# Performance work log

Hardware: AMD Instinct MI355X
Metric: run time of the kernel (lower is better)

The kernel has to match this reference:

```python
import jax, jax.numpy as jnp
from jax import lax
import numpy as np

# Problem dims (see init_kwargs)
B, CIN, H, W = 4, 128, 128, 128
COUT, K, STRIDE, PAD, DIL, GROUPS, OG = 128, 3, 1, 1, 1, 1, 2


def setup_inputs() -> dict:
    key = jax.random.key(0)
    k0, k1, k2 = jax.random.split(key, 3)
    x = jax.random.normal(k0, (B, CIN, H, W), dtype=jnp.float32)
    off_ch = 3 * OG * K * K  # with_mask=True -> scale=3 (dy, dx, mask)
    # Small random offset-conv weights so offsets are non-trivial (zero-init would degenerate to plain conv)
    w_off = jax.random.normal(k1, (off_ch, CIN, K, K), dtype=jnp.float32) * 0.01
    b_off = jnp.zeros((off_ch,), jnp.float32)
    stdv = 1.0 / np.sqrt(CIN * K * K)
    weight = jax.random.uniform(k2, (COUT, CIN // GROUPS, K, K), jnp.float32, -stdv, stdv)
    bias = jnp.zeros((COUT,), jnp.float32)
    return {"x": x, "w_off": w_off, "b_off": b_off, "weight": weight, "bias": bias}


def _deform_conv2d(x, offset, mask, weight, bias):
    # x: [B,C,H,W]; offset: [B,2*OG*K2,Ho,Wo]; mask: [B,OG*K2,Ho,Wo]
    Bn, C, Hn, Wn = x.shape
    O = weight.shape[0]
    K2 = K * K
    Ho = (Hn + 2 * PAD - DIL * (K - 1) - 1) // STRIDE + 1
    Wo = (Wn + 2 * PAD - DIL * (K - 1) - 1) // STRIDE + 1
    # torchvision layout: per offset group, per kernel point, (dy, dx) interleaved
    off = offset.reshape(Bn, OG, K2, 2, Ho, Wo)
    kg = (jnp.arange(K) * DIL).astype(x.dtype)
    kyf = jnp.repeat(kg, K)  # [K2] kernel row offset, k2 = i*K + j
    kxf = jnp.tile(kg, K)    # [K2] kernel col offset
    base_y = (jnp.arange(Ho) * STRIDE - PAD).astype(x.dtype)
    base_x = (jnp.arange(Wo) * STRIDE - PAD).astype(x.dtype)
    # sampling coords: [B,OG,K2,Ho,Wo]
    sy = base_y[None, None, None, :, None] + kyf[None, None, :, None, None] + off[:, :, :, 0]
    sx = base_x[None, None, None, None, :] + kxf[None, None, :, None, None] + off[:, :, :, 1]
    y0f = jnp.floor(sy)
    x0f = jnp.floor(sx)
    ly = sy - y0f  # bilinear fractional weights
    lx = sx - x0f
    y0 = y0f.astype(jnp.int32)
    x0 = x0f.astype(jnp.int32)
    Cg = C // OG
    xg = x.reshape(Bn, OG, Cg, Hn * Wn)

    def gather(iy, ix):
        # zero-padding semantics: out-of-range corners contribute 0
        valid = ((iy >= 0) & (iy < Hn) & (ix >= 0) & (ix < Wn)).astype(x.dtype)
        idx = (jnp.clip(iy, 0, Hn - 1) * Wn + jnp.clip(ix, 0, Wn - 1)).reshape(Bn, OG, 1, -1)
        v = jnp.take_along_axis(xg, idx, axis=3).reshape(Bn, OG, Cg, K2, Ho, Wo)
        return v * valid[:, :, None]

    v00 = gather(y0, x0)
    v01 = gather(y0, x0 + 1)
    v10 = gather(y0 + 1, x0)
    v11 = gather(y0 + 1, x0 + 1)
    wy = ly[:, :, None]  # broadcast over channel dim
    wx = lx[:, :, None]
    val = (v00 * (1 - wy) * (1 - wx) + v01 * (1 - wy) * wx
           + v10 * wy * (1 - wx) + v11 * wy * wx)
    # modulated DCNv2: multiply sampled values by sigmoid mask
    val = val * mask.reshape(Bn, OG, 1, K2, Ho, Wo)
    # im2col GEMM: cols [B,G,(C/G)*K2,Ho*Wo] x weight [G,O/G,(C/G)*K2]
    cols = val.reshape(Bn, GROUPS, (C // GROUPS) * K2, Ho * Wo)
    wg = weight.reshape(GROUPS, O // GROUPS, (C // GROUPS) * K2)
    out = jnp.einsum('gok,bgkn->bgon', wg, cols).reshape(Bn, O, Ho, Wo)
    return out + bias[None, :, None, None]


def reference(x, w_off, b_off, weight, bias):
    off_out = lax.conv_general_dilated(
        x, w_off, (STRIDE, STRIDE), [(PAD, PAD), (PAD, PAD)],
        rhs_dilation=(DIL, DIL), dimension_numbers=('NCHW', 'OIHW', 'NCHW')
    ) + b_off[None, :, None, None]
    oh, ow, m = jnp.split(off_out, 3, axis=1)
    offset = jnp.concatenate([oh, ow], axis=1)
    mask = jax.nn.sigmoid(m)
    return _deform_conv2d(x, offset, mask, weight, bias)
```

## Files before the change

### kernel.cpp

```cpp
#include <hip/hip_runtime.h>
#include <math.h>

#define NB 4
#define NC 128
#define NH 128
#define NW 128
#define NHW (NH*NW)
#define NCOUT 128

#define SY_OFF 0
#define SX_OFF 1179648
#define MK_OFF 2359296
#define WOFF_OFF 3538944
#define WMAIN_OFF 3580416
#define XT_OFF 3663360

typedef short short8 __attribute__((ext_vector_type(8)));
typedef float f32x4 __attribute__((ext_vector_type(4)));
typedef float f32x2 __attribute__((ext_vector_type(2)));

__device__ inline short f2bf(float f) {
    unsigned u = __float_as_uint(f);
    u = (u + 0x7FFFu + ((u >> 16) & 1u)) >> 16;
    return (short)u;
}
__device__ inline unsigned pack2(float lo, float hi) {
    unsigned r;
    asm("v_cvt_pk_bf16_f32 %0, %1, %2" : "=v"(r) : "v"(lo), "v"(hi));
    return r;
}
__device__ inline unsigned pkf16(float a, float b) {
    auto h = __builtin_amdgcn_cvt_pkrtz(a, b);
    unsigned r; __builtin_memcpy(&r, &h, 4); return r;
}
__device__ inline float f16f(unsigned s) {
    unsigned short us = (unsigned short)s;
    __fp16 h; __builtin_memcpy(&h, &us, 2); return (float)h;
}
__device__ inline f32x2 pkmul(f32x2 a, f32x2 b) {
    f32x2 d; asm("v_pk_mul_f32 %0, %1, %2" : "=v"(d) : "v"(a), "v"(b)); return d;
}
__device__ inline f32x2 pkfma(f32x2 a, f32x2 b, f32x2 c) {
    f32x2 d; asm("v_pk_fma_f32 %0, %1, %2, %3" : "=v"(d) : "v"(a), "v"(b), "v"(c)); return d;
}
__device__ inline f32x2 cpair(unsigned u) {
    f32x2 c; c.x = __uint_as_float(u << 16); c.y = __uint_as_float(u); return c;
}
__device__ inline void gload_lds16(const void* g, void* l) {
    __builtin_amdgcn_global_load_lds(
        (const __attribute__((address_space(1))) unsigned int*)g,
        (__attribute__((address_space(3))) unsigned int*)l, 16, 0, 0);
}

__global__ void wtrans_kernel(const float* __restrict__ w_off,
                              const float* __restrict__ weight,
                              float* __restrict__ ws)
{
    int i = blockIdx.x * 256 + threadIdx.x;
    if (i < 36*2304) {
        int s = i / 2304, rem = i - s*2304;
        int row = rem / 36, c = rem - row*36;
        int chunk = s / 9, k2 = s - 9*chunk;
        float v = (row < 54 && c < 32) ? w_off[(row*NC + chunk*32 + c)*9 + k2] : 0.f;
        ((short*)(ws + WOFF_OFF))[i] = f2bf(v);
    } else if (i < 36*2304 + 36*4608) {
        int j = i - 36*2304;
        int s = j / 4608, rem = j - s*4608;
        int row = rem / 36, c = rem - row*36;
        int chunk = s / 9, k2 = s - 9*chunk;
        float v = (c < 32) ? weight[(row*NC + chunk*32 + c)*9 + k2] : 0.f;
        ((short*)(ws + WMAIN_OFF))[j] = f2bf(v);
    }
}

__global__ __launch_bounds__(256) void xtrans_kernel(
    const float* __restrict__ x, float* __restrict__ ws)
{
    short* xT = (short*)(ws + XT_OFF);
    const int bid = blockIdx.x;
    const int ys = bid & 15, cg = (bid >> 4) & 15, b = bid >> 8;
    const int col = threadIdx.x & 127, rr = threadIdx.x >> 7;
    const float* xb = x + ((long)(b*NC + cg*8))*NHW;
#pragma unroll
    for (int yy = 0; yy < 4; ++yy) {
        const int y = ys*8 + yy*2 + rr;
        const float* p = xb + y*NW + col;
        float v[8];
#pragma unroll
        for (int q = 0; q < 8; ++q) v[q] = p[q*NHW];
        uint4 u = make_uint4(pack2(v[0],v[1]), pack2(v[2],v[3]),
                             pack2(v[4],v[5]), pack2(v[6],v[7]));
        *(uint4*)&xT[(((long)(b*16+cg)*NH + y)*NW + col)*8] = u;
    }
}

__global__ __launch_bounds__(512, 4) void offconv_kernel(
    float* __restrict__ ws, const float* __restrict__ b_off)
{
    __shared__ short wslab[2][2304];
    int bid = blockIdx.x;
    bid = (bid & 7) * 64 + (bid >> 3);
    const int b   = bid >> 7;
    const int ho  = bid & 127;
    const int tid = threadIdx.x;
    const int lane = tid & 63;
    const int wid = tid >> 6;
    const int n = lane & 15, g = lane >> 4;
    const int px = wid*16 + n;
    const short* woff = (const short*)(ws + WOFF_OFF);
    const char*  xTb  = (const char*)((const short*)(ws + XT_OFF) + (long)b*16*NHW*8);

    f32x4 acc[4];
#pragma unroll
    for (int rf = 0; rf < 4; ++rf) acc[rf] = (f32x4){0.f,0.f,0.f,0.f};

    auto DMA = [&](int it, int buf) {
        if (tid < 288) gload_lds16(woff + it*2304 + tid*8, &wslab[buf][tid*8]);
    };
    auto LOADB = [&](int it) -> short8 {
        const int chunk = it/9, k2 = it - 9*chunk;
        const int y = ho + k2/3 - 1, xc = px + (k2%3) - 1;
        short8 bf = (short8){0,0,0,0,0,0,0,0};
        if ((unsigned)y < NH && (unsigned)xc < NW)
            bf = *(const short8*)(xTb + ((long)(chunk*4 + g)*NHW + y*NW + xc)*16);
        return bf;
    };

    DMA(0, 0);
    short8 bcur = LOADB(0);
    asm volatile("s_waitcnt vmcnt(1) lgkmcnt(0)" ::: "memory");
    __builtin_amdgcn_s_barrier();
    __builtin_amdgcn_sched_barrier(0);

#pragma unroll 1
    for (int it = 0; it < 36; ++it) {
        const int cur = it & 1, nxt = cur ^ 1;
        short8 bnext;
        if (it < 35) { DMA(it+1, nxt); bnext = LOADB(it+1); }
        __builtin_amdgcn_sched_barrier(0);
#pragma unroll
        for (int rf = 0; rf < 4; ++rf) {
            short8 af = *(const short8*)&wslab[cur][(rf*16 + n)*36 + 8*g];
            acc[rf] = __builtin_amdgcn_mfma_f32_16x16x32_bf16(af, bcur, acc[rf], 0,0,0);
        }
        __builtin_amdgcn_sched_barrier(0);
        if (it < 35) {
            asm volatile("s_waitcnt vmcnt(1) lgkmcnt(0)" ::: "memory");
            __builtin_amdgcn_s_barrier();
            __builtin_amdgcn_sched_barrier(0);
        }
        bcur = bnext;
    }

#pragma unroll
    for (int rf = 0; rf < 4; ++rf) {
#pragma unroll
        for (int r = 0; r < 4; ++r) {
            int cout = 16*rf + 4*g + r;
            if (cout >= 54) continue;
            float v = acc[rf][r] + b_off[cout];
            if (cout < 36) {
                int og = cout / 18, rem = cout - 18*og;
                int k2c = rem >> 1, d = cout & 1;
                float base = d ? (float)(px - 1 + (k2c % 3))
                              : (float)(ho - 1 + (k2c / 3));
                ws[(d ? SX_OFF : SY_OFF) + (((b*2+og)*9 + k2c)*NHW) + ho*NW + px] = v + base;
            } else {
                int cc = cout - 36;
                int og = cc / 9, k2c = cc - 9*og;
                ws[MK_OFF + (((b*2+og)*9 + k2c)*NHW) + ho*NW + px] = 1.f/(1.f+expf(-v));
            }
        }
    }
}

__global__ __launch_bounds__(512, 4) void deform_kernel(
    float* __restrict__ ws, const float* __restrict__ bias,
    float* __restrict__ out)
{
    __shared__ short4 pI[18][128];
    __shared__ uint2  pWp[18][128];
    __shared__ short  wslab[2][4608];

    int bid = blockIdx.x;
    bid = (bid & 7) * 64 + (bid >> 3);
    const int b   = bid >> 7;
    const int ho  = bid & 127;
    const int tid = threadIdx.x;
    const int lane = tid & 63;
    const int wid = tid >> 6;
    const int n = lane & 15, g = lane >> 4;
    const int pxl = 16*wid + n;
    const short* wmn = (const short*)(ws + WMAIN_OFF);
    const char*  xTb = (const char*)((const short*)(ws + XT_OFF) + (long)b*16*NHW*8);

    f32x4 acc[8];
#pragma unroll
    for (int rf = 0; rf < 8; ++rf) acc[rf] = (f32x4){0.f,0.f,0.f,0.f};

    auto DMA = [&](int slabIdx, int buf) {
        const short* src = wmn + slabIdx*4608;
        gload_lds16(src + tid*8, &wslab[buf][tid*8]);
        if (tid < 64) gload_lds16(src + 4096 + tid*8, &wslab[buf][4096 + tid*8]);
    };

#define GLOAD(j, G0, G1, G2, G3) do {                                   \
        const int row_ = ((j)/18)*9 + (j)%9;                            \
        const int chunk_ = (j)/9;                                       \
        const short4 I_ = pI[row_][pxl];                                \
        const char* xp_ = xTb + (long)(chunk_*4 + g)*(NHW*16);          \
        G0 = *(const uint4*)(xp_ + (((int)I_.x) << 4));                 \
        G1 = *(const uint4*)(xp_ + (((int)I_.y) << 4));                 \
        G2 = *(const uint4*)(xp_ + (((int)I_.z) << 4));                 \
        G3 = *(const uint4*)(xp_ + (((int)I_.w) << 4));                 \
    } while (0)

#define FIN(j, G0, G1, G2, G3, Adst) do {                               \
        const int row_ = ((j)/18)*9 + (j)%9;                            \
        const uint2 wp_ = *(const uint2*)&pWp[row_][pxl];               \
        const float w0s = f16f(wp_.x), w1s = f16f(wp_.x >> 16);         \
        const float w2s = f16f(wp_.y), w3s = f16f(wp_.y >> 16);         \
        const f32x2 W0_ = {w0s, w0s}, W1_ = {w1s, w1s};                 \
        const f32x2 W2_ = {w2s, w2s}, W3_ = {w3s, w3s};                 \
        uint4 u_; unsigned* up_ = (unsigned*)&u_;                       \
        const unsigned* a_ = (const unsigned*)&G0;                      \
        const unsigned* b_ = (const unsigned*)&G1;                      \
        const unsigned* c_ = (const unsigned*)&G2;                      \
        const unsigned* d_ = (const unsigned*)&G3;                      \
        _Pragma("unroll")                                               \
        for (int e = 0; e < 4; ++e) {                                   \
            f32x2 r_ = pkmul(cpair(d_[e]), W3_);                        \
            r_ = pkfma(cpair(c_[e]), W2_, r_);                          \
            r_ = pkfma(cpair(b_[e]), W1_, r_);                          \
            r_ = pkfma(cpair(a_[e]), W0_, r_);                          \
            up_[e] = pack2(r_.x, r_.y);                                 \
        }                                                               \
        __builtin_memcpy(&Adst, &u_, 16);                               \
    } while (0)

    DMA(0, 0);

    for (int e = tid; e < 2304; e += 512) {
        const int row = e >> 7, p = e & 127;
        const int og = row / 9, k2 = row - 9*og;
        const int sidx = (((b*2+og)*9 + k2)*NHW) + ho*NW + p;
        const float sy = ws[SY_OFF + sidx];
        const float sx = ws[SX_OFF + sidx];
        const float m  = ws[MK_OFF + sidx];
        const float y0f = floorf(sy), x0f = floorf(sx);
        const float ly = sy - y0f, lx = sx - x0f;
        const int y0 = (int)y0f, x0i = (int)x0f;
        const int y1 = y0 + 1, x1 = x0i + 1;
        const bool vy0 = (unsigned)y0 < NH, vy1 = (unsigned)y1 < NH;
        const bool vx0 = (unsigned)x0i < NW, vx1 = (unsigned)x1 < NW;
        const int cy0 = min(max(y0,0),NH-1), cy1 = min(max(y1,0),NH-1);
        const int cx0 = min(max(x0i,0),NW-1), cx1 = min(max(x1,0),NW-1);
        pI[row][p] = make_short4(
            (short)(cy0*NW + cx0), (short)(cy0*NW + cx1),
            (short)(cy1*NW + cx0), (short)(cy1*NW + cx1));
        const float W0 = (vy0 && vx0) ? (1.f-ly)*(1.f-lx)*m : 0.f;
        const float W1 = (vy0 && vx1) ? (1.f-ly)*lx*m       : 0.f;
        const float W2 = (vy1 && vx0) ? ly*(1.f-lx)*m       : 0.f;
        const float W3 = (vy1 && vx1) ? ly*lx*m             : 0.f;
        pWp[row][p] = make_uint2(pkf16(W0, W1), pkf16(W2, W3));
    }
    __syncthreads();

    uint4 Ga0, Ga1, Ga2, Ga3, Gb0, Gb1, Gb2, Gb3;
    short8 Acur, Anxt;
    GLOAD(0, Ga0, Ga1, Ga2, Ga3);
    FIN(0, Ga0, Ga1, Ga2, Ga3, Acur);
    GLOAD(1, Gb0, Gb1, Gb2, Gb3);

#define BODY(it, Ain, Aout, H0, H1, H2, H3, F0, F1, F2, F3) do {        \
        const int cur_ = (it) & 1, nxt_ = cur_ ^ 1;                     \
        if ((it) < 35) DMA((it)+1, nxt_);                               \
        if ((it) < 34) GLOAD((it)+2, F0, F1, F2, F3);                   \
        __builtin_amdgcn_sched_barrier(0);                              \
        _Pragma("unroll")                                               \
        for (int rf = 0; rf < 8; ++rf) {                                \
            short8 bf = *(const short8*)&wslab[cur_][(16*rf + n)*36 + 8*g]; \
            acc[rf] = __builtin_amdgcn_mfma_f32_16x16x32_bf16(Ain, bf, acc[rf], 0,0,0); \
        }                                                               \
        if ((it) < 35) FIN((it)+1, H0, H1, H2, H3, Aout);               \
        if ((it) < 34) {                                                \
            asm volatile("s_waitcnt vmcnt(4) lgkmcnt(0)" ::: "memory"); \
            __builtin_amdgcn_s_barrier();                               \
            __builtin_amdgcn_sched_barrier(0);                          \
        } else if ((it) == 34) {                                        \
            asm volatile("s_waitcnt vmcnt(0) lgkmcnt(0)" ::: "memory"); \
            __builtin_amdgcn_s_barrier();                               \
            __builtin_amdgcn_sched_barrier(0);                          \
        }                                                               \
    } while (0)

#pragma unroll 1
    for (int t = 0; t < 18; ++t) {
        BODY(2*t,     Acur, Anxt, Gb0, Gb1, Gb2, Gb3, Ga0, Ga1, Ga2, Ga3);
        BODY(2*t + 1, Anxt, Acur, Ga0, Ga1, Ga2, Ga3, Gb0, Gb1, Gb2, Gb3);
    }
#undef BODY
#undef GLOAD
#undef FIN

#pragma unroll
    for (int rf = 0; rf < 8; ++rf) {
        const int cout = 16*rf + n;
        const float bb = bias[cout];
        float4 o = make_float4(acc[rf][0]+bb, acc[rf][1]+bb,
                               acc[rf][2]+bb, acc[rf][3]+bb);
        *(float4*)&out[((b*NCOUT + cout)*NH + ho)*NW + 16*wid + 4*g] = o;
    }
}

extern "C" void kernel_launch(void* const* d_in, const int* in_sizes, int n_in,
                              void* d_out, int out_size, void* d_ws, size_t ws_size,
                              hipStream_t stream)
{
    const float* x      = (const float*)d_in[0];
    const float* w_off  = (const float*)d_in[1];
    const float* b_off  = (const float*)d_in[2];
    const float* weight = (const float*)d_in[3];
    const float* bias   = (const float*)d_in[4];
    float* out = (float*)d_out;
    float* ws  = (float*)d_ws;

    hipLaunchKernelGGL(wtrans_kernel, dim3(972), dim3(256), 0, stream,
                       w_off, weight, ws);
    hipLaunchKernelGGL(xtrans_kernel, dim3(1024), dim3(256), 0, stream,
                       x, ws);
    hipLaunchKernelGGL(offconv_kernel, dim3(NB*NH), dim3(512), 0, stream,
                       ws, b_off);
    hipLaunchKernelGGL(deform_kernel, dim3(NB*NH), dim3(512), 0, stream,
                       ws, bias, out);
}
```

Before: 94.94 us.

## Stage nine weight slabs per chunk and drop per-iteration barriers in deform kernel

The deform kernel now loads all nine weight slabs of a channel chunk into LDS at once, computes the bilinear indices and weights per offset group (9 rows) instead of all 18 upfront, and runs a fully unrolled nine-step MFMA loop with no block barriers inside a chunk. This removes the per-iteration barrier and waitcnt synchronisation of the old double-buffered slab pipeline. In exchange, LDS use grows a lot and occupancy is lowered to 2 blocks per CU. Weight loads are also exposed at chunk boundaries because they wait on vmcnt(0). The offset kernel swaps its hand-written waitcnt/barrier sequence for __syncthreads.

Measured after the change: 93.30 us. No clear change (-1.7%).

```diff
diff --git a/kernel.cpp b/kernel.cpp
--- a/kernel.cpp
+++ b/kernel.cpp
@@ -128,9 +128,7 @@
 
     DMA(0, 0);
     short8 bcur = LOADB(0);
-    asm volatile("s_waitcnt vmcnt(1) lgkmcnt(0)" ::: "memory");
-    __builtin_amdgcn_s_barrier();
-    __builtin_amdgcn_sched_barrier(0);
+    __syncthreads();
 
 #pragma unroll 1
     for (int it = 0; it < 36; ++it) {
@@ -143,12 +141,7 @@
             short8 af = *(const short8*)&wslab[cur][(rf*16 + n)*36 + 8*g];
             acc[rf] = __builtin_amdgcn_mfma_f32_16x16x32_bf16(af, bcur, acc[rf], 0,0,0);
         }
-        __builtin_amdgcn_sched_barrier(0);
-        if (it < 35) {
-            asm volatile("s_waitcnt vmcnt(1) lgkmcnt(0)" ::: "memory");
-            __builtin_amdgcn_s_barrier();
-            __builtin_amdgcn_sched_barrier(0);
-        }
+        __syncthreads();
         bcur = bnext;
     }
 
@@ -174,13 +167,13 @@
     }
 }
 
-__global__ __launch_bounds__(512, 4) void deform_kernel(
+__global__ __launch_bounds__(512, 2) void deform_kernel(
     float* __restrict__ ws, const float* __restrict__ bias,
     float* __restrict__ out)
 {
-    __shared__ short4 pI[18][128];
-    __shared__ uint2  pWp[18][128];
-    __shared__ short  wslab[2][4608];
+    __shared__ short4 pI[9][128];
+    __shared__ uint2  pWp[9][128];
+    __shared__ short  slabs[9][4608];
 
     int bid = blockIdx.x;
     bid = (bid & 7) * 64 + (bid >> 3);
@@ -198,26 +191,25 @@
 #pragma unroll
     for (int rf = 0; rf < 8; ++rf) acc[rf] = (f32x4){0.f,0.f,0.f,0.f};
 
-    auto DMA = [&](int slabIdx, int buf) {
-        const short* src = wmn + slabIdx*4608;
-        gload_lds16(src + tid*8, &wslab[buf][tid*8]);
-        if (tid < 64) gload_lds16(src + 4096 + tid*8, &wslab[buf][4096 + tid*8]);
+    auto DMAC = [&](int chunk) {
+        const short* src = wmn + chunk*9*4608;
+        short* dst = &slabs[0][0];
+#pragma unroll 1
+        for (int u = tid; u < 5184; u += 512)
+            gload_lds16(src + u*8, dst + u*8);
     };
 
-#define GLOAD(j, G0, G1, G2, G3) do {                                   \
-        const int row_ = ((j)/18)*9 + (j)%9;                            \
-        const int chunk_ = (j)/9;                                       \
-        const short4 I_ = pI[row_][pxl];                                \
-        const char* xp_ = xTb + (long)(chunk_*4 + g)*(NHW*16);          \
+#define GLOAD(chunk, k2, G0, G1, G2, G3) do {                           \
+        const short4 I_ = pI[(k2)][pxl];                                \
+        const char* xp_ = xTb + (long)((chunk)*4 + g)*(NHW*16);         \
         G0 = *(const uint4*)(xp_ + (((int)I_.x) << 4));                 \
         G1 = *(const uint4*)(xp_ + (((int)I_.y) << 4));                 \
         G2 = *(const uint4*)(xp_ + (((int)I_.z) << 4));                 \
         G3 = *(const uint4*)(xp_ + (((int)I_.w) << 4));                 \
     } while (0)
 
-#define FIN(j, G0, G1, G2, G3, Adst) do {                               \
-        const int row_ = ((j)/18)*9 + (j)%9;                            \
-        const uint2 wp_ = *(const uint2*)&pWp[row_][pxl];               \
+#define FIN(k2, G0, G1, G2, G3, Adst) do {                              \
+        const uint2 wp_ = *(const uint2*)&pWp[(k2)][pxl];               \
         const float w0s = f16f(wp_.x), w1s = f16f(wp_.x >> 16);         \
         const float w2s = f16f(wp_.y), w3s = f16f(wp_.y >> 16);         \
         const f32x2 W0_ = {w0s, w0s}, W1_ = {w1s, w1s};                 \
@@ -238,68 +230,78 @@
         __builtin_memcpy(&Adst, &u_, 16);                               \
     } while (0)
 
-    DMA(0, 0);
-
-    for (int e = tid; e < 2304; e += 512) {
-        const int row = e >> 7, p = e & 127;
-        const int og = row / 9, k2 = row - 9*og;
-        const int sidx = (((b*2+og)*9 + k2)*NHW) + ho*NW + p;
-        const float sy = ws[SY_OFF + sidx];
-        const float sx = ws[SX_OFF + sidx];
-        const float m  = ws[MK_OFF + sidx];
-        const float y0f = floorf(sy), x0f = floorf(sx);
-        const float ly = sy - y0f, lx = sx - x0f;
-        const int y0 = (int)y0f, x0i = (int)x0f;
-        const int y1 = y0 + 1, x1 = x0i + 1;
-        const bool vy0 = (unsigned)y0 < NH, vy1 = (unsigned)y1 < NH;
-        const bool vx0 = (unsigned)x0i < NW, vx1 = (unsigned)x1 < NW;
-        const int cy0 = min(max(y0,0),NH-1), cy1 = min(max(y1,0),NH-1);
-        const int cx0 = min(max(x0i,0),NW-1), cx1 = min(max(x1,0),NW-1);
-        pI[row][p] = make_short4(
-            (short)(cy0*NW + cx0), (short)(cy0*NW + cx1),
-            (short)(cy1*NW + cx0), (short)(cy1*NW + cx1));
-        const float W0 = (vy0 && vx0) ? (1.f-ly)*(1.f-lx)*m : 0.f;
-        const float W1 = (vy0 && vx1) ? (1.f-ly)*lx*m       : 0.f;
-        const float W2 = (vy1 && vx0) ? ly*(1.f-lx)*m       : 0.f;
-        const float W3 = (vy1 && vx1) ? ly*lx*m             : 0.f;
-        pWp[row][p] = make_uint2(pkf16(W0, W1), pkf16(W2, W3));
-    }
-    __syncthreads();
+#define MFMA8(Ain, k2) do {                                             \
+        _Pragma("unroll")                                               \
+        for (int rf = 0; rf < 8; ++rf) {                                \
+            short8 bf = *(const short8*)&slabs[(k2)][(16*rf + n)*36 + 8*g]; \
+            acc[rf] = __builtin_amdgcn_mfma_f32_16x16x32_bf16(Ain, bf, acc[rf], 0,0,0); \
+        }                                                               \
+    } while (0)
+
+#define PBODY(k2, chunk, Ain, Aout, H0,H1,H2,H3, F0,F1,F2,F3) do {      \
+        if ((k2) < 7) GLOAD(chunk, (k2)+2, F0, F1, F2, F3);             \
+        MFMA8(Ain, k2);                                                 \
+        if ((k2) < 8) FIN((k2)+1, H0, H1, H2, H3, Aout);                \
+    } while (0)
 
     uint4 Ga0, Ga1, Ga2, Ga3, Gb0, Gb1, Gb2, Gb3;
     short8 Acur, Anxt;
-    GLOAD(0, Ga0, Ga1, Ga2, Ga3);
-    FIN(0, Ga0, Ga1, Ga2, Ga3, Acur);
-    GLOAD(1, Gb0, Gb1, Gb2, Gb3);
-
-#define BODY(it, Ain, Aout, H0, H1, H2, H3, F0, F1, F2, F3) do {        \
-        const int cur_ = (it) & 1, nxt_ = cur_ ^ 1;                     \
-        if ((it) < 35) DMA((it)+1, nxt_);                               \
-        if ((it) < 34) GLOAD((it)+2, F0, F1, F2, F3);                   \
-        __builtin_amdgcn_sched_barrier(0);                              \
-        _Pragma("unroll")                                               \
-        for (int rf = 0; rf < 8; ++rf) {                                \
-            short8 bf = *(const short8*)&wslab[cur_][(16*rf + n)*36 + 8*g]; \
-            acc[rf] = __builtin_amdgcn_mfma_f32_16x16x32_bf16(Ain, bf, acc[rf], 0,0,0); \
-        }                                                               \
-        if ((it) < 35) FIN((it)+1, H0, H1, H2, H3, Aout);               \
-        if ((it) < 34) {                                                \
-            asm volatile("s_waitcnt vmcnt(4) lgkmcnt(0)" ::: "memory"); \
-            __builtin_amdgcn_s_barrier();                               \
-            __builtin_amdgcn_sched_barrier(0);                          \
-        } else if ((it) == 34) {                                        \
-            asm volatile("s_waitcnt vmcnt(0) lgkmcnt(0)" ::: "memory"); \
-            __builtin_amdgcn_s_barrier();                               \
-            __builtin_amdgcn_sched_barrier(0);                          \
-        }                                                               \
-    } while (0)
 
 #pragma unroll 1
-    for (int t = 0; t < 18; ++t) {
-        BODY(2*t,     Acur, Anxt, Gb0, Gb1, Gb2, Gb3, Ga0, Ga1, Ga2, Ga3);
-        BODY(2*t + 1, Anxt, Acur, Ga0, Ga1, Ga2, Ga3, Gb0, Gb1, Gb2, Gb3);
-    }
-#undef BODY
+    for (int og = 0; og < 2; ++og) {
+        if (og) __syncthreads();
+        DMAC(og*2);
+        for (int e = tid; e < 1152; e += 512) {
+            const int row = e >> 7, p = e & 127;
+            const int sidx = (((b*2+og)*9 + row)*NHW) + ho*NW + p;
+            const float sy = ws[SY_OFF + sidx];
+            const float sx = ws[SX_OFF + sidx];
+            const float m  = ws[MK_OFF + sidx];
+            const float y0f = floorf(sy), x0f = floorf(sx);
+            const float ly = sy - y0f, lx = sx - x0f;
+            const int y0 = (int)y0f, x0i = (int)x0f;
+            const int y1 = y0 + 1, x1 = x0i + 1;
+            const bool vy0 = (unsigned)y0 < NH, vy1 = (unsigned)y1 < NH;
+            const bool vx0 = (unsigned)x0i < NW, vx1 = (unsigned)x1 < NW;
+            const int cy0 = min(max(y0,0),NH-1), cy1 = min(max(y1,0),NH-1);
+            const int cx0 = min(max(x0i,0),NW-1), cx1 = min(max(x1,0),NW-1);
+            pI[row][p] = make_short4(
+                (short)(cy0*NW + cx0), (short)(cy0*NW + cx1),
+                (short)(cy1*NW + cx0), (short)(cy1*NW + cx1));
+            const float W0 = (vy0 && vx0) ? (1.f-ly)*(1.f-lx)*m : 0.f;
+            const float W1 = (vy0 && vx1) ? (1.f-ly)*lx*m       : 0.f;
+            const float W2 = (vy1 && vx0) ? ly*(1.f-lx)*m       : 0.f;
+            const float W3 = (vy1 && vx1) ? ly*lx*m             : 0.f;
+            pWp[row][p] = make_uint2(pkf16(W0, W1), pkf16(W2, W3));
+        }
+        __syncthreads();
+
+#pragma unroll 1
+        for (int cc = 0; cc < 2; ++cc) {
+            const int chunk = og*2 + cc;
+            if (cc) {
+                __syncthreads();
+                DMAC(chunk);
+                asm volatile("s_waitcnt vmcnt(0) lgkmcnt(0)" ::: "memory");
+                __builtin_amdgcn_s_barrier();
+                __builtin_amdgcn_sched_barrier(0);
+            }
+            GLOAD(chunk, 0, Ga0, Ga1, Ga2, Ga3);
+            FIN(0, Ga0, Ga1, Ga2, Ga3, Acur);
+            GLOAD(chunk, 1, Gb0, Gb1, Gb2, Gb3);
+            PBODY(0, chunk, Acur, Anxt, Gb0,Gb1,Gb2,Gb3, Ga0,Ga1,Ga2,Ga3);
+            PBODY(1, chunk, Anxt, Acur, Ga0,Ga1,Ga2,Ga3, Gb0,Gb1,Gb2,Gb3);
+            PBODY(2, chunk, Acur, Anxt, Gb0,Gb1,Gb2,Gb3, Ga0,Ga1,Ga2,Ga3);
+            PBODY(3, chunk, Anxt, Acur, Ga0,Ga1,Ga2,Ga3, Gb0,Gb1,Gb2,Gb3);
+            PBODY(4, chunk, Acur, Anxt, Gb0,Gb1,Gb2,Gb3, Ga0,Ga1,Ga2,Ga3);
+            PBODY(5, chunk, Anxt, Acur, Ga0,Ga1,Ga2,Ga3, Gb0,Gb1,Gb2,Gb3);
+            PBODY(6, chunk, Acur, Anxt, Gb0,Gb1,Gb2,Gb3, Ga0,Ga1,Ga2,Ga3);
+            PBODY(7, chunk, Anxt, Acur, Ga0,Ga1,Ga2,Ga3, Gb0,Gb1,Gb2,Gb3);
+            PBODY(8, chunk, Acur, Anxt, Gb0,Gb1,Gb2,Gb3, Ga0,Ga1,Ga2,Ga3);
+        }
+    }
+#undef PBODY
+#undef MFMA8
 #undef GLOAD
 #undef FIN
 
```
